# Performance work log

Hardware: AMD Instinct MI355X
Metric: run time of the kernel (lower is better)

## Reference

```python
import jax, jax.numpy as jnp
import numpy as np
from jax import lax

# Module hyperparameters (from init_kwargs)
H, W, T = 80, 96, 112   # full-resolution feature volume size
C = 16                  # in_channel
K = 3                   # kernel_size (box filter)
D = 3                   # correlation window count per axis
SF = 2                  # correlation stride (sf)
CC = 2 * C + K ** 3     # conv1 in/out channels = 59


def _resize_axis_linear_ac(x, axis, out_size):
    """1D linear resize along `axis` with align_corners=True semantics."""
    in_size = x.shape[axis]
    pos = jnp.arange(out_size, dtype=x.dtype) * ((in_size - 1) / (out_size - 1))
    i0 = jnp.clip(jnp.floor(pos).astype(jnp.int32), 0, in_size - 2)
    w1 = pos - i0.astype(x.dtype)
    shp = [1] * x.ndim
    shp[axis] = out_size
    w1 = w1.reshape(shp)
    x0 = jnp.take(x, i0, axis=axis)
    x1 = jnp.take(x, i0 + 1, axis=axis)
    return x0 * (1.0 - w1) + x1 * w1


def upsample_trilinear_ac(x, factor=2):
    # matches nn.Upsample(scale_factor=2, mode='trilinear', align_corners=True)
    for axis in (2, 3, 4):
        x = _resize_axis_linear_ac(x, axis, x.shape[axis] * factor)
    return x


def _grid_sample_3d_one(src, coords):
    """src [C,H,W,T], coords [3,H,W,T] in voxel units.
    Trilinear sampling, zeros padding, align_corners=True (matches grid_sample)."""
    Hs, Ws, Ts = src.shape[1], src.shape[2], src.shape[3]
    cx, cy, cz = coords[0], coords[1], coords[2]
    x0 = jnp.floor(cx); y0 = jnp.floor(cy); z0 = jnp.floor(cz)
    fx = cx - x0; fy = cy - y0; fz = cz - z0
    x0i = x0.astype(jnp.int32); y0i = y0.astype(jnp.int32); z0i = z0.astype(jnp.int32)
    out = jnp.zeros_like(src)
    for dx in (0, 1):
        for dy in (0, 1):
            for dz in (0, 1):
                ix = x0i + dx; iy = y0i + dy; iz = z0i + dz
                valid = (ix >= 0) & (ix < Hs) & (iy >= 0) & (iy < Ws) & (iz >= 0) & (iz < Ts)
                v = src[:, jnp.clip(ix, 0, Hs - 1), jnp.clip(iy, 0, Ws - 1), jnp.clip(iz, 0, Ts - 1)]
                w = (fx if dx else 1.0 - fx) * (fy if dy else 1.0 - fy) * (fz if dz else 1.0 - fz)
                out = out + jnp.where(valid, w, 0.0)[None] * v
    return out


def spatial_transform(src, flow):
    # src [B,C,H,W,T], flow [B,3,H,W,T] (voxel displacement)
    grid = jnp.stack(jnp.meshgrid(jnp.arange(H), jnp.arange(W), jnp.arange(T), indexing='ij')).astype(src.dtype)
    coords = grid[None] + flow  # [B,3,H,W,T]
    return jax.vmap(_grid_sample_3d_one)(src, coords)


def _box3(x, pad):
    """Depthwise 3x3x3 ones-kernel conv with zero padding `pad` (separable box sum)."""
    x = jnp.pad(x, ((0, 0), (0, 0), (pad, pad), (pad, pad), (pad, pad)))
    for axis in (2, 3, 4):
        n = x.shape[axis]
        x = (lax.slice_in_dim(x, 0, n - 2, axis=axis)
             + lax.slice_in_dim(x, 1, n - 1, axis=axis)
             + lax.slice_in_dim(x, 2, n, axis=axis))
    return x


def correlation3d(mov, fix):
    Bh, Ch, Hh, Wh, Th = mov.shape
    pm = _box3(mov, 1)           # [B,C,H,W,T]
    pf = _box3(fix, SF + 1)      # [B,C,H+2*SF,W+2*SF,T+2*SF]
    vols = []
    for i in range(D):
        for j in range(D):
            for k in range(D):
                crop = pf[:, :, i * SF:i * SF + Hh, j * SF:j * SF + Wh, k * SF:k * SF + Th]
                vols.append(jnp.sum(pm * crop, axis=1))  # channel reduce -> [B,H,W,T]
    return jnp.stack(vols, axis=1) / float(K ** 3)        # [B,27,H,W,T]


def conv3d(x, w, b):
    y = lax.conv_general_dilated(x, w, window_strides=(1, 1, 1),
                                 padding=((1, 1), (1, 1), (1, 1)),
                                 dimension_numbers=('NCDHW', 'OIDHW', 'NCDHW'))
    return y + b[None, :, None, None, None]


def setup_inputs() -> dict:
    key = jax.random.key(0)
    ks = jax.random.split(key, 10)
    f32 = jnp.float32
    def n(k, shape, s=0.05):
        return jax.random.normal(k, shape, f32) * s
    return {
        'x': jax.random.normal(ks[0], (1, C, H, W, T), f32),
        'y': jax.random.normal(ks[1], (1, C, H, W, T), f32),
        'flow': jax.random.normal(ks[2], (1, 3, H // 2, W // 2, T // 2), f32),
        'w1a': n(ks[3], (CC, CC, 3, 3, 3)), 'b1a': jnp.zeros((CC,), f32),
        'w1b': n(ks[4], (C, CC, 3, 3, 3)), 'b1b': jnp.zeros((C,), f32),
        'w2a': n(ks[5], (C, C, 3, 3, 3)), 'b2a': jnp.zeros((C,), f32),
        'w2b': n(ks[6], (C, C, 3, 3, 3)), 'b2b': jnp.zeros((C,), f32),
        'wf': n(ks[7], (3, C, 3, 3, 3), 1e-5), 'bf': jnp.zeros((3,), f32),
    }


def reference(x, y, flow, w1a, b1a, w1b, b1b, w2a, b2a, w2b, b2b, wf, bf):
    # in_flow=True, scale=True: upsample 2*flow trilinearly, warp x
    flow_up = upsample_trilinear_ac(flow * 2.0)          # [B,3,H,W,T]
    xw = spatial_transform(x, flow_up)                   # warped moving features
    corr = correlation3d(xw, y)                          # [B,27,H,W,T]
    stack = jnp.concatenate([xw, corr, y], axis=1)       # [B,59,H,W,T]
    h = jax.nn.relu(conv3d(conv3d(stack, w1a, b1a), w1b, b1b))
    res = jax.nn.relu(conv3d(conv3d(h, w2a, b2a), w2b, b2b))
    return conv3d(h + res, wf, bf)                       # [B,3,H,W,T]
```

## Files before the change

kernel.cpp:

```cpp
#include <hip/hip_runtime.h>
#include <hip/hip_bf16.h>
#include <cstddef>

typedef __hip_bfloat16 bf16;
typedef __attribute__((ext_vector_type(8))) short short8;
typedef __attribute__((ext_vector_type(4))) float f32x4;

constexpr int H = 80, W = 96, T = 112;
constexpr int N = H * W * T;
constexpr int WT = W * T;
constexpr int Hh = 40, Wh = 48, Th = 56;
constexpr int Nh = Hh * Wh * Th;
constexpr int PH = 84, PW = 100, PT = 116;
constexpr int NPF = PH * PW * PT;

static __device__ __forceinline__ float b2f(bf16 v) { return __bfloat162float(v); }
static __device__ __forceinline__ bf16  f2b(float v) { return __float2bfloat16(v); }
static __device__ __forceinline__ float us2f(unsigned short u) { return __uint_as_float(((unsigned)u) << 16); }

__global__ __launch_bounds__(256) void wbuild_kernel(const float* __restrict__ w, bf16* __restrict__ wb,
                                                     int COUT, int CIN, int KC_TOT, int NT_TOT)
{
    int idx = blockIdx.x * 256 + threadIdx.x;
    int total = 27 * KC_TOT * NT_TOT * 512;
    if (idx >= total) return;
    int j    = idx & 7;
    int lane = (idx >> 3) & 63;
    int rest = idx >> 9;
    int nt   = rest % NT_TOT; rest /= NT_TOT;
    int kc   = rest % KC_TOT;
    int tap  = rest / KC_TOT;
    int o    = nt * 16 + (lane & 15);
    int cin  = kc * 32 + (lane >> 4) * 8 + j;
    float val = (o < COUT && cin < CIN) ? w[((size_t)o * CIN + cin) * 27 + tap] : 0.f;
    wb[idx] = f2b(val);
}

__global__ __launch_bounds__(256) void bias_kernel(const float* __restrict__ b1a, const float* __restrict__ b1b,
                                                   const float* __restrict__ b2a, const float* __restrict__ b2b,
                                                   const float* __restrict__ bff, float* __restrict__ out)
{
    int i = threadIdx.x;
    if (i < 64)       out[i] = (i < 59) ? b1a[i] : 0.f;
    else if (i < 96)  { int j = i - 64;  out[i] = (j < 16) ? b1b[j] : 0.f; }
    else if (i < 128) { int j = i - 96;  out[i] = (j < 16) ? b2a[j] : 0.f; }
    else if (i < 160) { int j = i - 128; out[i] = (j < 16) ? b2b[j] : 0.f; }
    else if (i < 176) { int j = i - 160; out[i] = (j < 3)  ? bff[j] : 0.f; }
}

__global__ __launch_bounds__(256) void upsample_kernel(const float* __restrict__ flow,
                                                       float* __restrict__ flow_up)
{
    int idx = blockIdx.x * 256 + threadIdx.x;
    if (idx >= 3 * N) return;
    int c = idx / N, v = idx % N;
    int t = v % T; int hw = v / T; int w = hw % W; int h = hw / W;
    float ph = (float)h * ((float)(Hh - 1) / (float)(H - 1));
    float pw = (float)w * ((float)(Wh - 1) / (float)(W - 1));
    float pt = (float)t * ((float)(Th - 1) / (float)(T - 1));
    int i0 = min((int)ph, Hh - 2); float fh = ph - (float)i0;
    int j0 = min((int)pw, Wh - 2); float fw = pw - (float)j0;
    int k0 = min((int)pt, Th - 2); float ft = pt - (float)k0;
    const float* fp = flow + (size_t)c * Nh;
    auto L = [&](int a, int b, int d) -> float {
        return 2.0f * fp[((size_t)a * Wh + b) * Th + d];
    };
    float v000 = L(i0, j0, k0),     v001 = L(i0, j0, k0 + 1);
    float v010 = L(i0, j0 + 1, k0), v011 = L(i0, j0 + 1, k0 + 1);
    float v100 = L(i0 + 1, j0, k0),     v101 = L(i0 + 1, j0, k0 + 1);
    float v110 = L(i0 + 1, j0 + 1, k0), v111 = L(i0 + 1, j0 + 1, k0 + 1);
    float val = (1.f - fh) * ((1.f - fw) * ((1.f - ft) * v000 + ft * v001)
                            +        fw  * ((1.f - ft) * v010 + ft * v011))
              +        fh  * ((1.f - fw) * ((1.f - ft) * v100 + ft * v101)
                            +        fw  * ((1.f - ft) * v110 + ft * v111));
    flow_up[idx] = val;
}

__global__ __launch_bounds__(256) void warp_kernel(const float* __restrict__ x,
                                                   const float* __restrict__ flow_up,
                                                   bf16* __restrict__ xw)
{
    int v = blockIdx.x * 256 + threadIdx.x;
    if (v >= N) return;
    int t = v % T; int hw = v / T; int w = hw % W; int h = hw / W;
    float cx = (float)h + flow_up[v];
    float cy = (float)w + flow_up[N + v];
    float cz = (float)t + flow_up[2 * N + v];
    float fx0 = floorf(cx), fy0 = floorf(cy), fz0 = floorf(cz);
    float fx = cx - fx0, fy = cy - fy0, fz = cz - fz0;
    int ix = (int)fx0, iy = (int)fy0, iz = (int)fz0;

    float wc[8];
    int   oc[8];
    #pragma unroll
    for (int c8 = 0; c8 < 8; c8++) {
        int dx = (c8 >> 2) & 1, dy = (c8 >> 1) & 1, dz = c8 & 1;
        int ax = ix + dx, ay = iy + dy, az = iz + dz;
        bool ok = ((unsigned)ax < (unsigned)H) && ((unsigned)ay < (unsigned)W) && ((unsigned)az < (unsigned)T);
        float wt = (dx ? fx : 1.f - fx) * (dy ? fy : 1.f - fy) * (dz ? fz : 1.f - fz);
        wc[c8] = ok ? wt : 0.f;
        int cax = min(max(ax, 0), H - 1);
        int cay = min(max(ay, 0), W - 1);
        int caz = min(max(az, 0), T - 1);
        oc[c8] = (cax * W + cay) * T + caz;
    }
    #pragma unroll 1
    for (int c = 0; c < 16; c++) {
        const float* xp = x + (size_t)c * N;
        float s = 0.f;
        #pragma unroll
        for (int c8 = 0; c8 < 8; c8++) s += wc[c8] * xp[oc[c8]];
        xw[(size_t)c * N + v] = f2b(s);
    }
}

__global__ __launch_bounds__(256) void pm_kernel(const bf16* __restrict__ xw, bf16* __restrict__ pm)
{
    int idx = blockIdx.x * 256 + threadIdx.x;
    int ts = idx % 7;  int r = idx / 7;
    int w  = r % W;    r /= W;
    int h  = r % H;    int c = r / H;
    int t0 = ts * 16;

    float acc[16];
    #pragma unroll
    for (int k = 0; k < 16; k++) acc[k] = 0.f;

    const bf16* base = xw + (size_t)c * N;
    #pragma unroll
    for (int dh = -1; dh <= 1; dh++)
        #pragma unroll
        for (int dw = -1; dw <= 1; dw++) {
            int hh = h + dh, ww = w + dw;
            if (((unsigned)hh < (unsigned)H) && ((unsigned)ww < (unsigned)W)) {
                const unsigned short* rp = (const unsigned short*)(base + (size_t)(hh * W + ww) * T);
                float v[18];
                v[0] = (t0 > 0) ? us2f(rp[t0 - 1]) : 0.f;
                short8 cA = *(const short8*)(rp + t0);
                short8 cB = *(const short8*)(rp + t0 + 8);
                #pragma unroll
                for (int j = 0; j < 8; j++) v[1 + j] = us2f((unsigned short)cA[j]);
                #pragma unroll
                for (int j = 0; j < 8; j++) v[9 + j] = us2f((unsigned short)cB[j]);
                v[17] = (t0 + 16 < T) ? us2f(rp[t0 + 16]) : 0.f;
                #pragma unroll
                for (int k = 0; k < 16; k++) acc[k] += v[k] + v[k + 1] + v[k + 2];
            }
        }

    unsigned short ch[16];
    #pragma unroll
    for (int k = 0; k < 16; k++) { bf16 b = f2b(acc[k]); ch[k] = *(unsigned short*)&b; }
    uint4* dst = (uint4*)((unsigned short*)pm + (size_t)c * N + (size_t)(h * W + w) * T + t0);
    dst[0] = ((uint4*)ch)[0];
    dst[1] = ((uint4*)ch)[1];
}

__global__ __launch_bounds__(256) void pf_kernel(const float* __restrict__ y, bf16* __restrict__ pf)
{
    int idx = blockIdx.x * 256 + threadIdx.x;
    int ds = idx & 7;  int r = idx >> 3;
    int b  = r % PW;   r /= PW;
    int a  = r % PH;   int c = r / PH;
    int d0 = ds * 16;

    float acc[16];
    #pragma unroll
    for (int k = 0; k < 16; k++) acc[k] = 0.f;

    const float* base = y + (size_t)c * N;
    #pragma unroll
    for (int da = 0; da < 3; da++)
        #pragma unroll
        for (int db = 0; db < 3; db++) {
            int hh = a - 3 + da, ww = b - 3 + db;
            if (((unsigned)hh < (unsigned)H) && ((unsigned)ww < (unsigned)W)) {
                const float* rp = base + (size_t)(hh * W + ww) * T;
                float v[24];
                if (d0 >= 8) {
                    float4 a0 = *(const float4*)(rp + d0 - 8);
                    float4 a1 = *(const float4*)(rp + d0 - 4);
                    v[0] = a0.x; v[1] = a0.y; v[2] = a0.z; v[3] = a0.w;
                    v[4] = a1.x; v[5] = a1.y; v[6] = a1.z; v[7] = a1.w;
                } else {
                    #pragma unroll
                    for (int j = 0; j < 8; j++) v[j] = 0.f;
                }
                if (d0 <= 104) {
                    float4 b0 = *(const float4*)(rp + d0);
                    float4 b1 = *(const float4*)(rp + d0 + 4);
                    v[8]  = b0.x; v[9]  = b0.y; v[10] = b0.z; v[11] = b0.w;
                    v[12] = b1.x; v[13] = b1.y; v[14] = b1.z; v[15] = b1.w;
                } else {
                    #pragma unroll
                    for (int j = 8; j < 16; j++) v[j] = 0.f;
                }
                if (d0 <= 96) {
                    float4 c0 = *(const float4*)(rp + d0 + 8);
                    float4 c1 = *(const float4*)(rp + d0 + 12);
                    v[16] = c0.x; v[17] = c0.y; v[18] = c0.z; v[19] = c0.w;
                    v[20] = c1.x; v[21] = c1.y; v[22] = c1.z; v[23] = c1.w;
                } else {
                    #pragma unroll
                    for (int j = 16; j < 24; j++) v[j] = 0.f;
                }
                #pragma unroll
                for (int k = 0; k < 16; k++) acc[k] += v[k + 5] + v[k + 6] + v[k + 7];
            }
        }

    unsigned short ch[16];
    #pragma unroll
    for (int k = 0; k < 16; k++) { bf16 bb = f2b(acc[k]); ch[k] = *(unsigned short*)&bb; }
    uint2* dst = (uint2*)((unsigned short*)pf + (size_t)c * NPF + (size_t)(a * PW + b) * PT + d0);
    int nst = (d0 == 112) ? 1 : 4;
    #pragma unroll
    for (int k = 0; k < 4; k++) if (k < nst) dst[k] = ((uint2*)ch)[k];
}

__global__ __launch_bounds__(256) void corr_assemble_kernel(const bf16* __restrict__ pm,
                                                            const bf16* __restrict__ pf,
                                                            const bf16* __restrict__ xw,
                                                            const float* __restrict__ y,
                                                            bf16* __restrict__ stack)
{
    int v = blockIdx.x * 256 + threadIdx.x;
    if (v >= N) return;
    int t = v % T; int hw = v / T; int w = hw % W; int h = hw / W;

    float pmv[16];
    #pragma unroll
    for (int c = 0; c < 16; c++) pmv[c] = b2f(pm[(size_t)c * N + v]);

    float acc[27];
    #pragma unroll
    for (int i = 0; i < 27; i++) acc[i] = 0.f;

    const size_t pbase = ((size_t)h * PW + w) * PT + t;
    #pragma unroll 1
    for (int c = 0; c < 16; c++) {
        const bf16* pfc = pf + (size_t)c * NPF + pbase;
        float pv = pmv[c];
        #pragma unroll
        for (int i = 0; i < 3; i++)
            #pragma unroll
            for (int j = 0; j < 3; j++)
                #pragma unroll
                for (int k = 0; k < 3; k++)
                    acc[i * 9 + j * 3 + k] += pv * b2f(pfc[((size_t)(2 * i) * PW + 2 * j) * PT + 2 * k]);
    }

    unsigned short ch[64];
    #pragma unroll
    for (int c = 0; c < 16; c++) ch[c] = ((const unsigned short*)xw)[(size_t)c * N + v];
    #pragma unroll
    for (int i = 0; i < 27; i++) { bf16 b = f2b(acc[i] * (1.f / 27.f)); ch[16 + i] = *(unsigned short*)&b; }
    #pragma unroll
    for (int c = 0; c < 16; c++) { bf16 b = f2b(y[(size_t)c * N + v]); ch[43 + c] = *(unsigned short*)&b; }
    #pragma unroll
    for (int c = 59; c < 64; c++) ch[c] = 0;
    uint4* dst = (uint4*)((unsigned short*)stack + (size_t)v * 64);
    #pragma unroll
    for (int k = 0; k < 8; k++) dst[k] = ((uint4*)ch)[k];
}

__global__ __launch_bounds__(256) void corr_kernel(const bf16* __restrict__ pm, const bf16* __restrict__ pf,
                                                   bf16* __restrict__ corr_tmp)
{
    int v = blockIdx.x * 256 + threadIdx.x;
    if (v >= N) return;
    int t = v % T; int hw = v / T; int w = hw % W; int h = hw / W;
    float pmv[16];
    #pragma unroll
    for (int c = 0; c < 16; c++) pmv[c] = b2f(pm[(size_t)c * N + v]);
    #pragma unroll 1
    for (int i = 0; i < 3; i++)
    #pragma unroll 1
    for (int j = 0; j < 3; j++)
    #pragma unroll 1
    for (int k = 0; k < 3; k++) {
        size_t base = ((size_t)(2 * i + h) * PW + (2 * j + w)) * PT + (2 * k + t);
        float s = 0.f;
        #pragma unroll
        for (int c = 0; c < 16; c++) s += pmv[c] * b2f(pf[(size_t)c * NPF + base]);
        corr_tmp[(size_t)v * 28 + (i * 9 + j * 3 + k)] = f2b(s * (1.f / 27.f));
    }
}

__global__ __launch_bounds__(256) void assemble_kernel(const bf16* __restrict__ xw,
                                                       const bf16* __restrict__ corr_tmp,
                                                       const float* __restrict__ y,
                                                       bf16* __restrict__ stack)
{
    int v = blockIdx.x * 256 + threadIdx.x;
    if (v >= N) return;
    unsigned short ch[64];
    #pragma unroll
    for (int c = 0; c < 16; c++) ch[c] = ((const unsigned short*)xw)[(size_t)c * N + v];
    #pragma unroll
    for (int i = 0; i < 27; i++) ch[16 + i] = ((const unsigned short*)corr_tmp)[(size_t)v * 28 + i];
    #pragma unroll
    for (int c = 0; c < 16; c++) { bf16 b = f2b(y[(size_t)c * N + v]); ch[43 + c] = *(unsigned short*)&b; }
    #pragma unroll
    for (int c = 59; c < 64; c++) ch[c] = 0;
    uint4* dst = (uint4*)((unsigned short*)stack + (size_t)v * 64);
    #pragma unroll
    for (int k = 0; k < 8; k++) dst[k] = ((uint4*)ch)[k];
}

template <int CST_IN, int KC_TOT, int NT, int NT_TOT, int CST_OUT, bool RELU, int STORE>
__global__ __launch_bounds__(256, 3) void conv_lds(const bf16* __restrict__ in,
                                                   const bf16* __restrict__ wb,
                                                   const float* __restrict__ bias,
                                                   const bf16* __restrict__ aux,
                                                   void* __restrict__ out,
                                                   int kc_off, int nt_off)
{
    constexpr int KCP     = CST_IN / 32;
    constexpr int ASTRIDE = 80;
    constexpr int ZOFF    = 648 * ASTRIDE;
    __shared__ __align__(16) char smem[648 * ASTRIDE + 16];

    const int tid  = threadIdx.x;
    const int lane = tid & 63;
    const int n16  = lane & 15;
    const int q    = lane >> 4;
    const int wv   = tid >> 6;

    int bid = blockIdx.x;
    int cid = (bid & 7) * 420 + (bid >> 3);
    int t0  = (cid % 7) * 16;
    int rs  = cid / 7;
    int w0  = (rs % 24) * 4;
    int h0  = (rs / 24) * 4;
    const int h = h0 + wv;

    unsigned msk[4];
    #pragma unroll
    for (int m2 = 0; m2 < 4; ++m2) {
        int w = w0 + m2, t = t0 + n16;
        bool vh[3] = { h > 0, true, h < H - 1 };
        bool vw[3] = { w > 0, true, w < W - 1 };
        bool vt[3] = { t > 0, true, t < T - 1 };
        unsigned m = 0;
        #pragma unroll
        for (int tap = 0; tap < 27; ++tap)
            if (vh[tap / 9] && vw[(tap % 9) / 3] && vt[tap % 3]) m |= (1u << tap);
        msk[m2] = m;
    }

    f32x4 acc[4][NT];
    #pragma unroll
    for (int nt = 0; nt < NT; ++nt) {
        float bv = (STORE == 1) ? 0.f : bias[nt * 16 + n16];
        #pragma unroll
        for (int m2 = 0; m2 < 4; ++m2)
            #pragma unroll
            for (int r = 0; r < 4; ++r) acc[m2][nt][r] = bv;
    }

    if (tid < 4) *(int*)(smem + ZOFF + tid * 4) = 0;

    #pragma unroll 1
    for (int kcp = 0; kcp < KCP; ++kcp) {
        if (kcp > 0) __syncthreads();
        #pragma unroll 1
        for (int it = 0; it < 11; ++it) {
            int slot = it * 64 + (tid >> 2);
            if (slot < 648) {
                int hh = slot / 108, rm = slot - hh * 108;
                int ww = rm / 18,    tt = rm - ww * 18;
                int gh = min(max(h0 - 1 + hh, 0), H - 1);
                int gw = min(max(w0 - 1 + ww, 0), W - 1);
                int gt = min(max(t0 - 1 + tt, 0), T - 1);
                const char* gp = (const char*)in + (size_t)((gh * W + gw) * T + gt) * (CST_IN * 2)
                                 + kcp * 64 + (tid & 3) * 16;
                *(uint4*)(smem + slot * ASTRIDE + (tid & 3) * 16) = *(const uint4*)gp;
            }
        }
        __syncthreads();

        auto loadB = [&](int tap, short8 (&bv)[NT]) {
            #pragma unroll
            for (int nt = 0; nt < NT; ++nt) {
                size_t grec = (size_t)((tap * KC_TOT) + kcp + kc_off) * NT_TOT + nt + nt_off;
                bv[nt] = *(const short8*)((const char*)wb + grec * 1024 + (size_t)lane * 16);
            }
        };
        auto tapcompute = [&](int tap, short8 (&bv)[NT]) {
            int dh = tap / 9, rr = tap - dh * 9, dw = rr / 3, dt = rr - dw * 3;
            short8 av[4];
            #pragma unroll
            for (int m2 = 0; m2 < 4; ++m2) {
                bool ok = (msk[m2] >> tap) & 1u;
                int hvox = ((wv + dh) * 6 + (m2 + dw)) * 18 + (n16 + dt);
                const char* p = ok ? (smem + hvox * ASTRIDE + q * 16) : (smem + ZOFF);
                av[m2] = *(const short8*)p;
            }
            #pragma unroll
            for (int nt = 0; nt < NT; ++nt)
                #pragma unroll
                for (int m2 = 0; m2 < 4; ++m2)
                    acc[m2][nt] = __builtin_amdgcn_mfma_f32_16x16x32_bf16(av[m2], bv[nt], acc[m2][nt], 0, 0, 0);
        };

        short8 bvA[NT], bvB[NT];
        loadB(0, bvA);
        #pragma unroll 1
        for (int tap = 0; tap < 26; tap += 2) {
            loadB(tap + 1, bvB);
            tapcompute(tap, bvA);
            loadB(tap + 2, bvA);
            tapcompute(tap + 1, bvB);
        }
        tapcompute(26, bvA);
    }

    #pragma unroll
    for (int m2 = 0; m2 < 4; ++m2) {
        int vrow = (h * W + (w0 + m2)) * T + t0 + q * 4;
        #pragma unroll
        for (int r = 0; r < 4; ++r) {
            int v = vrow + r;
            #pragma unroll
            for (int nt = 0; nt < NT; ++nt) {
                float x = acc[m2][nt][r];
                if (STORE == 2 && nt == 0) x += b2f(aux[(size_t)v * 16 + n16]);
                if (RELU && STORE != 4) x = fmaxf(x, 0.f);
                if (STORE == 4) x = fmaxf(x, 0.f) + b2f(aux[(size_t)v * CST_OUT + nt * 16 + n16]);
                if (STORE == 1) {
                    if (nt == 0) ((bf16*)out)[(size_t)v * 16 + n16] = f2b(x);
                } else if (STORE == 3) {
                    int ch = nt * 16 + n16;
                    if (ch < 3) ((float*)out)[(size_t)ch * N + v] = x;
                } else {
                    ((bf16*)out)[(size_t)v * CST_OUT + nt * 16 + n16] = f2b(x);
                }
            }
        }
    }
}

extern "C" void kernel_launch(void* const* d_in, const int* in_sizes, int n_in,
                              void* d_out, int out_size, void* d_ws, size_t ws_size,
                              hipStream_t stream)
{
    (void)in_sizes; (void)n_in; (void)out_size;
    const float* x_p   = (const float*)d_in[0];
    const float* y_p   = (const float*)d_in[1];
    const float* flow_p= (const float*)d_in[2];
    const float* w1a_p = (const float*)d_in[3];
    const float* b1a_p = (const float*)d_in[4];
    const float* w1b_p = (const float*)d_in[5];
    const float* b1b_p = (const float*)d_in[6];
    const float* w2a_p = (const float*)d_in[7];
    const float* b2a_p = (const float*)d_in[8];
    const float* w2b_p = (const float*)d_in[9];
    const float* b2b_p = (const float*)d_in[10];
    const float* wf_p  = (const float*)d_in[11];
    const float* bf_p  = (const float*)d_in[12];

    char* wsb = (char*)d_ws;
    const size_t NB32 = (size_t)N * 32 * 2;
    const size_t NB64 = 2 * NB32;
    const size_t WSUM = (110592 + 55296 + 27648 + 27648 + 13824);
    const size_t NEED_BIG = 2 * NB64 + WSUM * 2 + 176 * 4 + 256;
    const bool BIG = (ws_size >= NEED_BIG);

    bf16 *stack, *buf1, *pm, *pf, *xw, *corr_tmp, *hbuf, *t2buf, *sumbuf, *hpart, *buf1h;
    float* flow_up; bf16* wroot;
    if (BIG) {
        stack    = (bf16*)wsb;
        flow_up  = (float*)wsb;
        hbuf     = (bf16*)wsb;
        t2buf    = (bf16*)(wsb + NB32);
        buf1     = (bf16*)(wsb + NB64);
        xw       = (bf16*)(wsb + NB64);
        pm       = (bf16*)(wsb + NB64 + (size_t)16 * N * 2);
        pf       = (bf16*)(wsb + NB64 + (size_t)32 * N * 2);
        sumbuf   = (bf16*)(wsb + NB64);
        corr_tmp = nullptr; hpart = nullptr; buf1h = nullptr;
        wroot    = (bf16*)(wsb + 2 * NB64);
    } else {
        const size_t A_off = 0, B_off = 2 * NB32, C_off = 3 * NB32;
        const size_t D_off = C_off + (size_t)N * 16 * 2;
        pf       = (bf16*)(wsb + A_off);
        pm       = (bf16*)(wsb + A_off + (size_t)16 * NPF * 2);
        flow_up  = (float*)(wsb + A_off + (size_t)16 * NPF * 2 + (size_t)16 * N * 2);
        stack    = (bf16*)(wsb + A_off);
        hbuf     = (bf16*)(wsb + A_off);
        t2buf    = (bf16*)(wsb + A_off + NB32);
        corr_tmp = (bf16*)(wsb + B_off);
        buf1h    = (bf16*)(wsb + B_off);
        sumbuf   = (bf16*)(wsb + B_off);
        xw       = (bf16*)(wsb + C_off);
        hpart    = (bf16*)(wsb + C_off);
        buf1     = nullptr;
        wroot    = (bf16*)(wsb + D_off);
    }
    bf16*  wb1a  = wroot;
    bf16*  wb1b  = wb1a + 110592;
    bf16*  wb2a  = wb1b + 55296;
    bf16*  wb2b  = wb2a + 27648;
    bf16*  wbf   = wb2b + 27648;
    float* biasp = (float*)(wbf + 13824);

    wbuild_kernel<<<432, 256, 0, stream>>>(w1a_p, wb1a, 59, 59, 2, 4);
    wbuild_kernel<<<216, 256, 0, stream>>>(w1b_p, wb1b, 16, 59, 2, 2);
    wbuild_kernel<<<108, 256, 0, stream>>>(w2a_p, wb2a, 16, 16, 1, 2);
    wbuild_kernel<<<108, 256, 0, stream>>>(w2b_p, wb2b, 16, 16, 1, 2);
    wbuild_kernel<<<54,  256, 0, stream>>>(wf_p,  wbf,  3,  16, 1, 1);
    bias_kernel<<<1, 256, 0, stream>>>(b1a_p, b1b_p, b2a_p, b2b_p, bf_p, biasp);

    upsample_kernel<<<3 * N / 256, 256, 0, stream>>>(flow_p, flow_up);
    warp_kernel<<<N / 256, 256, 0, stream>>>(x_p, flow_up, xw);
    pm_kernel<<<N / 256, 256, 0, stream>>>(xw, pm);
    pf_kernel<<<16 * PH * PW * 8 / 256, 256, 0, stream>>>(y_p, pf);
    if (BIG) {
        corr_assemble_kernel<<<N / 256, 256, 0, stream>>>(pm, pf, xw, y_p, stack);
    } else {
        corr_kernel<<<N / 256, 256, 0, stream>>>(pm, pf, corr_tmp);
        assemble_kernel<<<N / 256, 256, 0, stream>>>(xw, corr_tmp, y_p, stack);
    }

    const int GB = N / 256;
    if (BIG) {
        conv_lds<64, 2, 4, 4, 64, false, 0><<<GB, 256, 0, stream>>>(stack, wb1a, biasp + 0,   nullptr, buf1,  0, 0);
        conv_lds<64, 2, 2, 2, 32, true,  0><<<GB, 256, 0, stream>>>(buf1,  wb1b, biasp + 64,  nullptr, hbuf,  0, 0);
    } else {
        conv_lds<64, 2, 2, 4, 32, false, 0><<<GB, 256, 0, stream>>>(stack, wb1a, biasp + 0,   nullptr, buf1h, 0, 0);
        conv_lds<32, 2, 2, 2, 32, false, 1><<<GB, 256, 0, stream>>>(buf1h, wb1b, biasp,       nullptr, hpart, 0, 0);
        conv_lds<64, 2, 2, 4, 32, false, 0><<<GB, 256, 0, stream>>>(stack, wb1a, biasp + 32,  nullptr, buf1h, 0, 2);
        conv_lds<32, 2, 2, 2, 32, true,  2><<<GB, 256, 0, stream>>>(buf1h, wb1b, biasp + 64,  hpart,   hbuf,  1, 0);
    }
    conv_lds<32, 1, 2, 2, 32, false, 0><<<GB, 256, 0, stream>>>(hbuf,  wb2a, biasp + 96,  nullptr, t2buf,  0, 0);
    conv_lds<32, 1, 2, 2, 32, false, 4><<<GB, 256, 0, stream>>>(t2buf, wb2b, biasp + 128, hbuf,    sumbuf, 0, 0);
    conv_lds<32, 1, 1, 1, 16, false, 3><<<GB, 256, 0, stream>>>(sumbuf, wbf, biasp + 160, nullptr, d_out,  0, 0);
}
```

Measured before the change: 987.0 us.

## Specialize conv kernel for interior tiles and fully unroll tap loop

Adds a compile-time split between interior tiles, which skip the per-tap boundary mask and zero-pointer select, and border tiles, which keep the masked path. The 27-tap loop is now fully unrolled with constant LDS offsets from a precomputed base pointer, and weight loads use precomputed strides instead of the manual double-buffered loadB scheme. This cuts address arithmetic and predication in the inner MFMA loop. In exchange it doubles the code size, and full unrolling may raise register pressure or lose the explicit prefetch overlap of weight loads.

```diff
diff --git a/kernel.cpp b/kernel.cpp
--- a/kernel.cpp
+++ b/kernel.cpp
@@ -1,6 +1,7 @@
 #include <hip/hip_runtime.h>
 #include <hip/hip_bf16.h>
 #include <cstddef>
+#include <type_traits>
 
 typedef __hip_bfloat16 bf16;
 typedef __attribute__((ext_vector_type(8))) short short8;
@@ -335,19 +336,8 @@
     int h0  = (rs / 24) * 4;
     const int h = h0 + wv;
 
-    unsigned msk[4];
-    #pragma unroll
-    for (int m2 = 0; m2 < 4; ++m2) {
-        int w = w0 + m2, t = t0 + n16;
-        bool vh[3] = { h > 0, true, h < H - 1 };
-        bool vw[3] = { w > 0, true, w < W - 1 };
-        bool vt[3] = { t > 0, true, t < T - 1 };
-        unsigned m = 0;
-        #pragma unroll
-        for (int tap = 0; tap < 27; ++tap)
-            if (vh[tap / 9] && vw[(tap % 9) / 3] && vt[tap % 3]) m |= (1u << tap);
-        msk[m2] = m;
-    }
+    const bool interior = (h0 != 0) && (h0 != H - 4) && (w0 != 0) && (w0 != W - 4)
+                       && (t0 != 0) && (t0 != T - 16);
 
     f32x4 acc[4][NT];
     #pragma unroll
@@ -361,60 +351,80 @@
 
     if (tid < 4) *(int*)(smem + ZOFF + tid * 4) = 0;
 
-    #pragma unroll 1
-    for (int kcp = 0; kcp < KCP; ++kcp) {
-        if (kcp > 0) __syncthreads();
-        #pragma unroll 1
-        for (int it = 0; it < 11; ++it) {
-            int slot = it * 64 + (tid >> 2);
-            if (slot < 648) {
-                int hh = slot / 108, rm = slot - hh * 108;
-                int ww = rm / 18,    tt = rm - ww * 18;
-                int gh = min(max(h0 - 1 + hh, 0), H - 1);
-                int gw = min(max(w0 - 1 + ww, 0), W - 1);
-                int gt = min(max(t0 - 1 + tt, 0), T - 1);
-                const char* gp = (const char*)in + (size_t)((gh * W + gw) * T + gt) * (CST_IN * 2)
-                                 + kcp * 64 + (tid & 3) * 16;
-                *(uint4*)(smem + slot * ASTRIDE + (tid & 3) * 16) = *(const uint4*)gp;
+    const char* abase = smem + (size_t)(wv * 108 + n16) * ASTRIDE + q * 16;
+
+    auto run = [&](auto chk_c) {
+        constexpr bool CHK = decltype(chk_c)::value;
+        unsigned msk[4];
+        if (CHK) {
+            #pragma unroll
+            for (int m2 = 0; m2 < 4; ++m2) {
+                int w = w0 + m2, t = t0 + n16;
+                bool vh[3] = { h > 0, true, h < H - 1 };
+                bool vw[3] = { w > 0, true, w < W - 1 };
+                bool vt[3] = { t > 0, true, t < T - 1 };
+                unsigned m = 0;
+                #pragma unroll
+                for (int tap = 0; tap < 27; ++tap)
+                    if (vh[tap / 9] && vw[(tap % 9) / 3] && vt[tap % 3]) m |= (1u << tap);
+                msk[m2] = m;
             }
         }
-        __syncthreads();
-
-        auto loadB = [&](int tap, short8 (&bv)[NT]) {
+
+        #pragma unroll 1
+        for (int kcp = 0; kcp < KCP; ++kcp) {
+            if (kcp > 0) __syncthreads();
+            #pragma unroll 1
+            for (int it = 0; it < 11; ++it) {
+                int slot = it * 64 + (tid >> 2);
+                if (slot < 648) {
+                    int hh = slot / 108, rm = slot - hh * 108;
+                    int ww = rm / 18,    tt = rm - ww * 18;
+                    int gh = min(max(h0 - 1 + hh, 0), H - 1);
+                    int gw = min(max(w0 - 1 + ww, 0), W - 1);
+                    int gt = min(max(t0 - 1 + tt, 0), T - 1);
+                    const char* gp = (const char*)in + (size_t)((gh * W + gw) * T + gt) * (CST_IN * 2)
+                                     + kcp * 64 + (tid & 3) * 16;
+                    *(uint4*)(smem + slot * ASTRIDE + (tid & 3) * 16) = *(const uint4*)gp;
+                }
+            }
+            __syncthreads();
+
+            const char* wbk = (const char*)wb
+                            + ((size_t)(kcp + kc_off) * NT_TOT + nt_off) * 1024
+                            + (size_t)lane * 16;
+
             #pragma unroll
-            for (int nt = 0; nt < NT; ++nt) {
-                size_t grec = (size_t)((tap * KC_TOT) + kcp + kc_off) * NT_TOT + nt + nt_off;
-                bv[nt] = *(const short8*)((const char*)wb + grec * 1024 + (size_t)lane * 16);
+            for (int tap = 0; tap < 27; ++tap) {
+                short8 bv[NT];
+                #pragma unroll
+                for (int nt = 0; nt < NT; ++nt)
+                    bv[nt] = *(const short8*)(wbk + (size_t)tap * (KC_TOT * NT_TOT * 1024) + nt * 1024);
+
+                int dh = tap / 9, rr = tap - dh * 9, dw = rr / 3, dt = rr - dw * 3;
+                short8 av[4];
+                #pragma unroll
+                for (int m2 = 0; m2 < 4; ++m2) {
+                    int boff = ((dh * 6 + m2 + dw) * 18 + dt) * ASTRIDE;
+                    const char* p;
+                    if (CHK) {
+                        bool ok = (msk[m2] >> tap) & 1u;
+                        p = ok ? (abase + boff) : (smem + ZOFF);
+                    } else {
+                        p = abase + boff;
+                    }
+                    av[m2] = *(const short8*)p;
+                }
+                #pragma unroll
+                for (int nt = 0; nt < NT; ++nt)
+                    #pragma unroll
+                    for (int m2 = 0; m2 < 4; ++m2)
+                        acc[m2][nt] = __builtin_amdgcn_mfma_f32_16x16x32_bf16(av[m2], bv[nt], acc[m2][nt], 0, 0, 0);
             }
-        };
-        auto tapcompute = [&](int tap, short8 (&bv)[NT]) {
-            int dh = tap / 9, rr = tap - dh * 9, dw = rr / 3, dt = rr - dw * 3;
-            short8 av[4];
-            #pragma unroll
-            for (int m2 = 0; m2 < 4; ++m2) {
-                bool ok = (msk[m2] >> tap) & 1u;
-                int hvox = ((wv + dh) * 6 + (m2 + dw)) * 18 + (n16 + dt);
-                const char* p = ok ? (smem + hvox * ASTRIDE + q * 16) : (smem + ZOFF);
-                av[m2] = *(const short8*)p;
-            }
-            #pragma unroll
-            for (int nt = 0; nt < NT; ++nt)
-                #pragma unroll
-                for (int m2 = 0; m2 < 4; ++m2)
-                    acc[m2][nt] = __builtin_amdgcn_mfma_f32_16x16x32_bf16(av[m2], bv[nt], acc[m2][nt], 0, 0, 0);
-        };
-
-        short8 bvA[NT], bvB[NT];
-        loadB(0, bvA);
-        #pragma unroll 1
-        for (int tap = 0; tap < 26; tap += 2) {
-            loadB(tap + 1, bvB);
-            tapcompute(tap, bvA);
-            loadB(tap + 2, bvA);
-            tapcompute(tap + 1, bvB);
         }
-        tapcompute(26, bvA);
-    }
+    };
+    if (interior) run(std::integral_constant<bool, false>{});
+    else          run(std::integral_constant<bool, true>{});
 
     #pragma unroll
     for (int m2 = 0; m2 < 4; ++m2) {
```

Measured after the change: 1.193 ms. 1.21x slower.
